# Optimization experiments

Measured on AMD Instinct MI355X. Metric: run time of the kernel, lower is better.

The kernel has to match this reference:

```python
import jax, jax.numpy as jnp
import numpy as np

N_NODES = 100000
N_EDGES = 1600000
N_GRAPHS = 512
F_IN = 20
HID = 128
OUT = HID // 2


def _glorot(key, shape):
    fan_in, fan_out = shape[0], shape[1]
    lim = float(np.sqrt(6.0 / (fan_in + fan_out)))
    return jax.random.uniform(key, shape, jnp.float32, -lim, lim)


def setup_inputs() -> dict:
    key = jax.random.key(0)
    ks = jax.random.split(key, 12)
    x = jax.random.normal(ks[0], (N_NODES, F_IN), jnp.float32)
    edge_index = jax.random.randint(ks[1], (2, N_EDGES), 0, N_NODES, dtype=jnp.int64)
    batch = jnp.sort(jax.random.randint(ks[2], (N_NODES,), 0, N_GRAPHS, dtype=jnp.int64))
    return {
        "x": x,
        "edge_index": edge_index,
        "batch": batch,
        "W1": _glorot(ks[3], (F_IN, HID)), "b1": jnp.zeros((HID,), jnp.float32),
        "W2": _glorot(ks[4], (HID, HID)), "b2": jnp.zeros((HID,), jnp.float32),
        "W3": _glorot(ks[5], (HID, HID)), "b3": jnp.zeros((HID,), jnp.float32),
        "Wout": _glorot(ks[6], (HID, OUT)), "bout": jnp.zeros((OUT,), jnp.float32),
    }


def _gcn_conv(x, W, b, src, dst, num_nodes):
    # PyG GCNConv: x' = D^{-1/2} (A + I) D^{-1/2} X W + b (self-loops already in src/dst)
    xw = x @ W                                                  # [N, H]
    ones = jnp.ones(src.shape[0], dtype=xw.dtype)
    deg = jax.ops.segment_sum(ones, dst, num_segments=num_nodes)
    dinv = jnp.where(deg > 0, jax.lax.rsqrt(deg), 0.0)          # [N]
    norm = dinv[src] * dinv[dst]                                # [E+N]
    msg = xw[src] * norm[:, None]                               # gather + scale
    return jax.ops.segment_sum(msg, dst, num_segments=num_nodes) + b


def reference(x, edge_index, batch, W1, b1, W2, b2, W3, b3, Wout, bout):
    num_nodes = x.shape[0]
    loops = jnp.arange(num_nodes, dtype=edge_index.dtype)
    src = jnp.concatenate([edge_index[0], loops])
    dst = jnp.concatenate([edge_index[1], loops])

    h = jax.nn.relu(_gcn_conv(x, W1, b1, src, dst, num_nodes))
    h = jax.nn.relu(_gcn_conv(h, W2, b2, src, dst, num_nodes))
    h = jax.nn.relu(_gcn_conv(h, W3, b3, src, dst, num_nodes))

    # global_mean_pool over graph ids
    sums = jax.ops.segment_sum(h, batch, num_segments=N_GRAPHS)
    counts = jax.ops.segment_sum(jnp.ones(num_nodes, h.dtype), batch, num_segments=N_GRAPHS)
    pooled = sums / jnp.maximum(counts, 1.0)[:, None]           # [G, H]
    return pooled @ Wout + bout                                 # [G, H//2]
```

## Files before the change

kernel.cpp:

```cpp
#include <hip/hip_runtime.h>
#include <hip/hip_fp16.h>

#define N_NODES 100000
#define N_EDGES 1600000
#define N_GRAPHS 512
#define F_IN 20
#define HID 128
#define OUT_F 64

#define BUCKETS 256
#define SPAN 391
#define BCAP 7000
#define EPB 2048

typedef _Float16 half8_t __attribute__((ext_vector_type(8)));
typedef float f32x4_t __attribute__((ext_vector_type(4)));

__device__ inline float4 h4_to_f4(uint2 u) {
    __half2 h0 = *(__half2*)&u.x;
    __half2 h1 = *(__half2*)&u.y;
    float2 f0 = __half22float2(h0);
    float2 f1 = __half22float2(h1);
    return make_float4(f0.x, f0.y, f1.x, f1.y);
}

__global__ void zero_all(float* sums, float* counts, int* cur256) {
    int i = blockIdx.x * 256 + threadIdx.x;
    sums[i] = 0.f;
    if (i < N_GRAPHS) counts[i] = 0.f;
    if (i >= 512 && i < 512 + BUCKETS) cur256[i - 512] = 0;
}

__global__ __launch_bounds__(256) void partition(const int* __restrict__ src,
                                                 const int* __restrict__ dst,
                                                 int* __restrict__ bpairs,
                                                 int* cur256) {
    __shared__ int lcnt[BUCKETS];
    __shared__ int lbase[BUCKETS];
    int t = threadIdx.x;
    lcnt[t] = 0;
    __syncthreads();
    int base = blockIdx.x * EPB;
    int myb[8], myp[8];
#pragma unroll
    for (int i = 0; i < 8; ++i) {
        int e = base + i * 256 + t;
        int b = -1, p = 0;
        if (e < N_EDGES) {
            int s = src[e], d = dst[e];
            b = d / SPAN;
            p = (s << 9) | (d - b * SPAN);
            atomicAdd(&lcnt[b], 1);
        }
        myb[i] = b; myp[i] = p;
    }
    __syncthreads();
    lbase[t] = atomicAdd(&cur256[t], lcnt[t]);
    lcnt[t] = 0;
    __syncthreads();
#pragma unroll
    for (int i = 0; i < 8; ++i) {
        int b = myb[i];
        if (b >= 0) {
            int p = lbase[b] + atomicAdd(&lcnt[b], 1);
            if (p < BCAP) bpairs[(size_t)b * BCAP + p] = myp[i];
        }
    }
}

__global__ void scan_bbase(const int* __restrict__ cur256, int* bbase, int* row_st) {
    __shared__ int sc[BUCKETS];
    int t = threadIdx.x;
    int v = cur256[t];
    sc[t] = v;
    __syncthreads();
    for (int o = 1; o < BUCKETS; o <<= 1) {
        int x = (t >= o) ? sc[t - o] : 0;
        __syncthreads();
        sc[t] += x;
        __syncthreads();
    }
    bbase[t] = sc[t] - v;
    if (t == 0) row_st[N_NODES] = N_EDGES;
}

__global__ __launch_bounds__(256) void csr_build(const int* __restrict__ bpairs,
                                                 const int* __restrict__ bcnt,
                                                 const int* __restrict__ bbase,
                                                 int* __restrict__ row_st,
                                                 int* __restrict__ csr) {
    __shared__ int ocnt[SPAN];
    __shared__ int sc[512];
    __shared__ int cur[SPAN];
    int b = blockIdx.x, t = threadIdx.x;
    int n0 = b * SPAN;
    int span = N_NODES - n0; if (span > SPAN) span = SPAN;
    for (int i = t; i < SPAN; i += 256) ocnt[i] = 0;
    __syncthreads();
    int n = bcnt[b];
    const int* p = bpairs + (size_t)b * BCAP;
    for (int i = t; i < n; i += 256) atomicAdd(&ocnt[p[i] & 511], 1);
    __syncthreads();
    sc[t]       = (t < span) ? ocnt[t] : 0;
    sc[t + 256] = (t + 256 < span) ? ocnt[t + 256] : 0;
    __syncthreads();
    for (int o = 1; o < 512; o <<= 1) {
        int a0 = (t >= o) ? sc[t - o] : 0;
        int a1 = sc[t + 256 - o];
        __syncthreads();
        sc[t] += a0;
        sc[t + 256] += a1;
        __syncthreads();
    }
    int base = bbase[b];
    for (int i = t; i < span; i += 256) {
        int start = sc[i] - ocnt[i];
        row_st[n0 + i] = base + start;
        cur[i] = start;
    }
    __syncthreads();
    for (int i = t; i < n; i += 256) {
        int e = p[i];
        int lp = atomicAdd(&cur[e & 511], 1);
        csr[base + lp] = e >> 9;
    }
}

__global__ void scale_x(const float* __restrict__ x, const int* __restrict__ row_st,
                        __half* __restrict__ Xs) {
    int i = blockIdx.x * 256 + threadIdx.x;
    int n = i >> 5, f = i & 31;
    if (n >= N_NODES) return;
    float v = (f < F_IN) ? x[n * F_IN + f] : 0.f;
    float di = rsqrtf((float)(row_st[n + 1] - row_st[n] + 1));
    Xs[i] = __float2half(di * v);
}

__global__ __launch_bounds__(256) void gather20(const __half* __restrict__ Xs,
                                                const int* __restrict__ row_st,
                                                const int* __restrict__ csr,
                                                float* __restrict__ Xagg) {
    int t = threadIdx.x;
    if (t >= 240) return;
    int g = t / F_IN, f = t % F_IN;
    int n = blockIdx.x * 12 + g;
    if (n >= N_NODES) return;
    int r0 = row_st[n], r1 = row_st[n + 1];
    float acc = __half2float(Xs[n * 32 + f]);
    int r = r0;
    for (; r + 3 < r1; r += 4) {
        int s0 = csr[r], s1 = csr[r + 1], s2 = csr[r + 2], s3 = csr[r + 3];
        float v0 = __half2float(Xs[s0 * 32 + f]);
        float v1 = __half2float(Xs[s1 * 32 + f]);
        float v2 = __half2float(Xs[s2 * 32 + f]);
        float v3 = __half2float(Xs[s3 * 32 + f]);
        acc += (v0 + v1) + (v2 + v3);
    }
    for (; r < r1; ++r) acc += __half2float(Xs[csr[r] * 32 + f]);
    float di = rsqrtf((float)(r1 - r0 + 1));
    Xagg[n * F_IN + f] = di * acc;
}

__global__ __launch_bounds__(256) void gemm_l1(const float* __restrict__ A,
                                               const float* __restrict__ W,
                                               const float* __restrict__ bias,
                                               __half* __restrict__ C) {
    __shared__ float Alds[16 * F_IN];
    __shared__ float Wlds[F_IN * HID];
    const int t = threadIdx.x;
    const int node0 = blockIdx.x * 16;

    for (int idx = t; idx < 16 * F_IN; idx += 256)
        Alds[idx] = A[node0 * F_IN + idx];
    for (int idx = t; idx < F_IN * HID; idx += 256)
        Wlds[idx] = W[idx];
    __syncthreads();

    const int h4 = (t & 31) * 4;
    const int g  = t >> 5;
    float4 b4 = *(const float4*)&bias[h4];
    float4 acc0 = b4;
    float4 acc1 = b4;
#pragma unroll
    for (int kk = 0; kk < F_IN; ++kk) {
        float a0 = Alds[(g * 2) * F_IN + kk];
        float a1 = Alds[(g * 2 + 1) * F_IN + kk];
        float4 w = *(const float4*)&Wlds[kk * HID + h4];
        acc0.x = fmaf(a0, w.x, acc0.x);
        acc0.y = fmaf(a0, w.y, acc0.y);
        acc0.z = fmaf(a0, w.z, acc0.z);
        acc0.w = fmaf(a0, w.w, acc0.w);
        acc1.x = fmaf(a1, w.x, acc1.x);
        acc1.y = fmaf(a1, w.y, acc1.y);
        acc1.z = fmaf(a1, w.z, acc1.z);
        acc1.w = fmaf(a1, w.w, acc1.w);
    }
    {
        __half2 h0 = __floats2half2_rn(acc0.x, acc0.y);
        __half2 h1 = __floats2half2_rn(acc0.z, acc0.w);
        uint2 u; u.x = *(unsigned*)&h0; u.y = *(unsigned*)&h1;
        ((uint2*)C)[(node0 + g * 2) * 32 + (h4 >> 2)] = u;
    }
    {
        __half2 h0 = __floats2half2_rn(acc1.x, acc1.y);
        __half2 h1 = __floats2half2_rn(acc1.z, acc1.w);
        uint2 u; u.x = *(unsigned*)&h0; u.y = *(unsigned*)&h1;
        ((uint2*)C)[(node0 + g * 2 + 1) * 32 + (h4 >> 2)] = u;
    }
}

__global__ __launch_bounds__(256) void gemm_mfma(const __half* __restrict__ H,
                                                 const float* __restrict__ W,
                                                 const int* __restrict__ row_st,
                                                 __half* __restrict__ T) {
    __shared__ _Float16 Whi[128 * 128];
    __shared__ _Float16 Wlo[128 * 128];
    const int t = threadIdx.x;

    for (int i = t; i < 128 * 128; i += 256) {
        int k = i >> 7, c = i & 127;
        float w = W[i];
        _Float16 hi = (_Float16)w;
        _Float16 lo = (_Float16)((w - (float)hi) * 2048.0f);
        int addr = c * 128 + (((k >> 3) ^ (c & 15)) << 3) + (k & 7);
        Whi[addr] = hi;
        Wlo[addr] = lo;
    }
    __syncthreads();

    const int wv = t >> 6;
    const int l  = t & 63;
    const int lr = l & 15;
    const int lq = l >> 4;

    for (int rep = 0; rep < 4; ++rep) {
        int strip = (blockIdx.x * 4 + wv) * 4 + rep;
        if (strip >= N_NODES / 16) continue;
        int n0 = strip * 16;

        f32x4_t acc[8], acl[8];
#pragma unroll
        for (int ct = 0; ct < 8; ++ct) { acc[ct] = (f32x4_t){0,0,0,0}; acl[ct] = (f32x4_t){0,0,0,0}; }

#pragma unroll
        for (int kc = 0; kc < 4; ++kc) {
            half8_t a = *(const half8_t*)(H + (size_t)(n0 + lr) * 128 + kc * 32 + lq * 8);
#pragma unroll
            for (int j = 0; j < 8; ++j) a[j] = a[j] > (_Float16)0 ? a[j] : (_Float16)0;
            int g = kc * 4 + lq;
#pragma unroll
            for (int ct = 0; ct < 8; ++ct) {
                int c = ct * 16 + lr;
                int addr = c * 128 + ((g ^ lr) << 3);
                half8_t bh = *(const half8_t*)&Whi[addr];
                half8_t bl = *(const half8_t*)&Wlo[addr];
                acc[ct] = __builtin_amdgcn_mfma_f32_16x16x32_f16(a, bh, acc[ct], 0, 0, 0);
                acl[ct] = __builtin_amdgcn_mfma_f32_16x16x32_f16(a, bl, acl[ct], 0, 0, 0);
            }
        }

        int r0 = n0 + lq * 4;
#pragma unroll
        for (int r = 0; r < 4; ++r) {
            int row = r0 + r;
            float d = rsqrtf((float)(row_st[row + 1] - row_st[row] + 1));
#pragma unroll
            for (int ct = 0; ct < 8; ++ct) {
                float v = (acc[ct][r] + acl[ct][r] * 4.8828125e-4f) * d;
                T[(size_t)row * 128 + ct * 16 + lr] = __float2half(v);
            }
        }
    }
}

__global__ __launch_bounds__(256) void gather_range(const __half* __restrict__ A,
                                                    const int* __restrict__ row_st,
                                                    const int* __restrict__ csr,
                                                    const float* __restrict__ bias,
                                                    __half* __restrict__ B) {
    int t = threadIdx.x;
    int n = blockIdx.x * 8 + (t >> 5);
    int l = t & 31;
    int r0 = row_st[n], r1 = row_st[n + 1];
    float di = rsqrtf((float)(r1 - r0 + 1));
    const uint2* Af = (const uint2*)A;
    float4 acc = h4_to_f4(Af[n * 32 + l]);
    int r = r0;
    for (; r + 3 < r1; r += 4) {
        int s0 = csr[r];
        int s1 = csr[r + 1];
        int s2 = csr[r + 2];
        int s3 = csr[r + 3];
        float4 v0 = h4_to_f4(Af[s0 * 32 + l]);
        float4 v1 = h4_to_f4(Af[s1 * 32 + l]);
        float4 v2 = h4_to_f4(Af[s2 * 32 + l]);
        float4 v3 = h4_to_f4(Af[s3 * 32 + l]);
        acc.x += (v0.x + v1.x) + (v2.x + v3.x);
        acc.y += (v0.y + v1.y) + (v2.y + v3.y);
        acc.z += (v0.z + v1.z) + (v2.z + v3.z);
        acc.w += (v0.w + v1.w) + (v2.w + v3.w);
    }
    for (; r < r1; ++r) {
        float4 v = h4_to_f4(Af[csr[r] * 32 + l]);
        acc.x += v.x; acc.y += v.y; acc.z += v.z; acc.w += v.w;
    }
    float4 b4 = ((const float4*)bias)[l];
    __half2 h0 = __floats2half2_rn(fmaf(di, acc.x, b4.x), fmaf(di, acc.y, b4.y));
    __half2 h1 = __floats2half2_rn(fmaf(di, acc.z, b4.z), fmaf(di, acc.w, b4.w));
    uint2 u; u.x = *(unsigned*)&h0; u.y = *(unsigned*)&h1;
    ((uint2*)B)[n * 32 + l] = u;
}

__global__ __launch_bounds__(256) void pool(const __half* __restrict__ B,
                                            const int* __restrict__ batch,
                                            float* sums, float* counts) {
    int t = threadIdx.x;
    int grp = blockIdx.x * 8 + (t >> 5);
    int l = t & 31;
    int h4 = l * 4;
    int n0 = grp * 8;
    if (n0 >= N_NODES) return;
    const uint2* Bf = (const uint2*)B;
    int cur = batch[n0];
    int runlen = 0;
    float4 acc = make_float4(0.f, 0.f, 0.f, 0.f);
    for (int k = 0; k < 8; ++k) {
        int n = n0 + k;
        if (n >= N_NODES) break;
        int g = batch[n];
        if (g != cur) {
            float* sp = &sums[cur * HID + h4];
            atomicAdd(sp + 0, acc.x); atomicAdd(sp + 1, acc.y);
            atomicAdd(sp + 2, acc.z); atomicAdd(sp + 3, acc.w);
            if (l == 0) atomicAdd(&counts[cur], (float)runlen);
            acc = make_float4(0.f, 0.f, 0.f, 0.f);
            runlen = 0;
            cur = g;
        }
        float4 v = h4_to_f4(Bf[n * 32 + l]);
        acc.x += fmaxf(v.x, 0.f);
        acc.y += fmaxf(v.y, 0.f);
        acc.z += fmaxf(v.z, 0.f);
        acc.w += fmaxf(v.w, 0.f);
        ++runlen;
    }
    float* sp = &sums[cur * HID + h4];
    atomicAdd(sp + 0, acc.x); atomicAdd(sp + 1, acc.y);
    atomicAdd(sp + 2, acc.z); atomicAdd(sp + 3, acc.w);
    if (l == 0) atomicAdd(&counts[cur], (float)runlen);
}

__global__ void final_gemm(const float* __restrict__ sums, const float* __restrict__ counts,
                           const float* __restrict__ Wout, const float* __restrict__ bout,
                           float* __restrict__ out) {
    int g = blockIdx.x;
    int o = threadIdx.x;
    __shared__ float p[HID];
    for (int k = o; k < HID; k += 64) p[k] = sums[g * HID + k];
    __syncthreads();
    float inv = 1.0f / fmaxf(counts[g], 1.0f);
    float acc = 0.f;
#pragma unroll 8
    for (int k = 0; k < HID; ++k)
        acc = fmaf(p[k], Wout[k * OUT_F + o], acc);
    out[g * OUT_F + o] = fmaf(inv, acc, bout[o]);
}

extern "C" void kernel_launch(void* const* d_in, const int* in_sizes, int n_in,
                              void* d_out, int out_size, void* d_ws, size_t ws_size,
                              hipStream_t stream) {
    const float* x     = (const float*)d_in[0];
    const int*   ei    = (const int*)d_in[1];
    const int*   batch = (const int*)d_in[2];
    const float* W1    = (const float*)d_in[3];
    const float* b1    = (const float*)d_in[4];
    const float* W2    = (const float*)d_in[5];
    const float* b2    = (const float*)d_in[6];
    const float* W3    = (const float*)d_in[7];
    const float* b3    = (const float*)d_in[8];
    const float* Wout  = (const float*)d_in[9];
    const float* bout  = (const float*)d_in[10];
    float* out = (float*)d_out;

    const int* src = ei;
    const int* dst = ei + N_EDGES;

    float* A      = (float*)d_ws;
    float* Breg   = A + (size_t)N_NODES * HID;
    int*   row_st = (int*)(Breg + (size_t)N_NODES * HID);
    float* sums   = (float*)(row_st + N_NODES + 1);
    float* counts = sums + N_GRAPHS * HID;
    int*   csr    = (int*)(counts + N_GRAPHS);
    int*   cur256 = csr + N_EDGES;
    int*   bbase  = cur256 + BUCKETS;

    int*    bpairs = (int*)A;
    __half* Xs     = (__half*)A;
    float*  Xagg   = A + 1600000;
    __half* T      = (__half*)A;
    __half* H      = (__half*)Breg;

    zero_all<<<N_GRAPHS * HID / 256, 256, 0, stream>>>(sums, counts, cur256);
    partition<<<(N_EDGES + EPB - 1) / EPB, 256, 0, stream>>>(src, dst, bpairs, cur256);
    scan_bbase<<<1, BUCKETS, 0, stream>>>(cur256, bbase, row_st);
    csr_build<<<BUCKETS, 256, 0, stream>>>(bpairs, cur256, bbase, row_st, csr);

    scale_x<<<N_NODES * 32 / 256, 256, 0, stream>>>(x, row_st, Xs);
    gather20<<<(N_NODES + 11) / 12, 256, 0, stream>>>(Xs, row_st, csr, Xagg);
    gemm_l1<<<N_NODES / 16, 256, 0, stream>>>(Xagg, W1, b1, H);

    gemm_mfma<<<391, 256, 0, stream>>>(H, W2, row_st, T);
    gather_range<<<N_NODES / 8, 256, 0, stream>>>(T, row_st, csr, b2, H);
    gemm_mfma<<<391, 256, 0, stream>>>(H, W3, row_st, T);
    gather_range<<<N_NODES / 8, 256, 0, stream>>>(T, row_st, csr, b3, H);

    pool<<<(N_NODES / 8 + 7) / 8, 256, 0, stream>>>(H, batch, sums, counts);
    final_gemm<<<N_GRAPHS, 64, 0, stream>>>(sums, counts, Wout, bout, out);
}
```

Measured before the change: 401.0 us.

## Fuse layer-1 gather into GEMM, per-wave partition counters, unroll gather by 8

Merges the 20-feature neighbor gather and the first-layer GEMM into one kernel, so the aggregated features stay in LDS and no longer round-trip through global memory. Partition now keeps a separate bucket counter per wavefront and takes each edge's rank from the first atomic, which removes the second pass of LDS atomics. The 128-wide gather loop is unrolled to 8 neighbors to put more loads in flight, and the zeroing kernel is replaced by hipMemsetAsync calls. The risks are higher register pressure from the unroll and a gather in layer1 that now uses 32 lanes per node while only 20 of them produce results.

```diff
diff --git a/kernel.cpp b/kernel.cpp
--- a/kernel.cpp
+++ b/kernel.cpp
@@ -24,45 +24,45 @@
     return make_float4(f0.x, f0.y, f1.x, f1.y);
 }
 
-__global__ void zero_all(float* sums, float* counts, int* cur256) {
-    int i = blockIdx.x * 256 + threadIdx.x;
-    sums[i] = 0.f;
-    if (i < N_GRAPHS) counts[i] = 0.f;
-    if (i >= 512 && i < 512 + BUCKETS) cur256[i - 512] = 0;
-}
-
 __global__ __launch_bounds__(256) void partition(const int* __restrict__ src,
                                                  const int* __restrict__ dst,
                                                  int* __restrict__ bpairs,
                                                  int* cur256) {
-    __shared__ int lcnt[BUCKETS];
-    __shared__ int lbase[BUCKETS];
+    __shared__ int lcnt[4][BUCKETS];
+    __shared__ int woff[4][BUCKETS];
     int t = threadIdx.x;
-    lcnt[t] = 0;
+    int wv = t >> 6;
+    for (int i = t; i < 4 * BUCKETS; i += 256) ((int*)lcnt)[i] = 0;
     __syncthreads();
     int base = blockIdx.x * EPB;
-    int myb[8], myp[8];
+    int myb[8], myp[8], myr[8];
 #pragma unroll
     for (int i = 0; i < 8; ++i) {
         int e = base + i * 256 + t;
-        int b = -1, p = 0;
+        int b = -1, p = 0, rk = 0;
         if (e < N_EDGES) {
             int s = src[e], d = dst[e];
             b = d / SPAN;
             p = (s << 9) | (d - b * SPAN);
-            atomicAdd(&lcnt[b], 1);
-        }
-        myb[i] = b; myp[i] = p;
-    }
-    __syncthreads();
-    lbase[t] = atomicAdd(&cur256[t], lcnt[t]);
-    lcnt[t] = 0;
+            rk = atomicAdd(&lcnt[wv][b], 1);
+        }
+        myb[i] = b; myp[i] = p; myr[i] = rk;
+    }
+    __syncthreads();
+    {
+        int c0 = lcnt[0][t], c1 = lcnt[1][t], c2 = lcnt[2][t], c3 = lcnt[3][t];
+        int gb = atomicAdd(&cur256[t], c0 + c1 + c2 + c3);
+        woff[0][t] = gb;
+        woff[1][t] = gb + c0;
+        woff[2][t] = gb + c0 + c1;
+        woff[3][t] = gb + c0 + c1 + c2;
+    }
     __syncthreads();
 #pragma unroll
     for (int i = 0; i < 8; ++i) {
         int b = myb[i];
         if (b >= 0) {
-            int p = lbase[b] + atomicAdd(&lcnt[b], 1);
+            int p = woff[wv][b] + myr[i];
             if (p < BCAP) bpairs[(size_t)b * BCAP + p] = myp[i];
         }
     }
@@ -136,44 +136,37 @@
     Xs[i] = __float2half(di * v);
 }
 
-__global__ __launch_bounds__(256) void gather20(const __half* __restrict__ Xs,
-                                                const int* __restrict__ row_st,
-                                                const int* __restrict__ csr,
-                                                float* __restrict__ Xagg) {
-    int t = threadIdx.x;
-    if (t >= 240) return;
-    int g = t / F_IN, f = t % F_IN;
-    int n = blockIdx.x * 12 + g;
-    if (n >= N_NODES) return;
-    int r0 = row_st[n], r1 = row_st[n + 1];
-    float acc = __half2float(Xs[n * 32 + f]);
-    int r = r0;
-    for (; r + 3 < r1; r += 4) {
-        int s0 = csr[r], s1 = csr[r + 1], s2 = csr[r + 2], s3 = csr[r + 3];
-        float v0 = __half2float(Xs[s0 * 32 + f]);
-        float v1 = __half2float(Xs[s1 * 32 + f]);
-        float v2 = __half2float(Xs[s2 * 32 + f]);
-        float v3 = __half2float(Xs[s3 * 32 + f]);
-        acc += (v0 + v1) + (v2 + v3);
-    }
-    for (; r < r1; ++r) acc += __half2float(Xs[csr[r] * 32 + f]);
-    float di = rsqrtf((float)(r1 - r0 + 1));
-    Xagg[n * F_IN + f] = di * acc;
-}
-
-__global__ __launch_bounds__(256) void gemm_l1(const float* __restrict__ A,
-                                               const float* __restrict__ W,
-                                               const float* __restrict__ bias,
-                                               __half* __restrict__ C) {
+__global__ __launch_bounds__(256) void layer1(const __half* __restrict__ Xs,
+                                              const int* __restrict__ row_st,
+                                              const int* __restrict__ csr,
+                                              const float* __restrict__ W,
+                                              const float* __restrict__ bias,
+                                              __half* __restrict__ H) {
+    __shared__ float Wlds[F_IN * HID];
     __shared__ float Alds[16 * F_IN];
-    __shared__ float Wlds[F_IN * HID];
     const int t = threadIdx.x;
     const int node0 = blockIdx.x * 16;
 
-    for (int idx = t; idx < 16 * F_IN; idx += 256)
-        Alds[idx] = A[node0 * F_IN + idx];
-    for (int idx = t; idx < F_IN * HID; idx += 256)
-        Wlds[idx] = W[idx];
+    for (int i = t; i < F_IN * HID; i += 256) Wlds[i] = W[i];
+
+    const int hw = t >> 5, l = t & 31;
+    for (int k = 0; k < 2; ++k) {
+        int nn = node0 + hw * 2 + k;
+        int r0 = row_st[nn], r1 = row_st[nn + 1];
+        float acc = __half2float(Xs[nn * 32 + l]);
+        int r = r0;
+        for (; r + 3 < r1; r += 4) {
+            int s0 = csr[r], s1 = csr[r + 1], s2 = csr[r + 2], s3 = csr[r + 3];
+            float v0 = __half2float(Xs[s0 * 32 + l]);
+            float v1 = __half2float(Xs[s1 * 32 + l]);
+            float v2 = __half2float(Xs[s2 * 32 + l]);
+            float v3 = __half2float(Xs[s3 * 32 + l]);
+            acc += (v0 + v1) + (v2 + v3);
+        }
+        for (; r < r1; ++r) acc += __half2float(Xs[csr[r] * 32 + l]);
+        float di = rsqrtf((float)(r1 - r0 + 1));
+        if (l < F_IN) Alds[(hw * 2 + k) * F_IN + l] = di * acc;
+    }
     __syncthreads();
 
     const int h4 = (t & 31) * 4;
@@ -199,13 +192,13 @@
         __half2 h0 = __floats2half2_rn(acc0.x, acc0.y);
         __half2 h1 = __floats2half2_rn(acc0.z, acc0.w);
         uint2 u; u.x = *(unsigned*)&h0; u.y = *(unsigned*)&h1;
-        ((uint2*)C)[(node0 + g * 2) * 32 + (h4 >> 2)] = u;
+        ((uint2*)H)[(node0 + g * 2) * 32 + (h4 >> 2)] = u;
     }
     {
         __half2 h0 = __floats2half2_rn(acc1.x, acc1.y);
         __half2 h1 = __floats2half2_rn(acc1.z, acc1.w);
         uint2 u; u.x = *(unsigned*)&h0; u.y = *(unsigned*)&h1;
-        ((uint2*)C)[(node0 + g * 2 + 1) * 32 + (h4 >> 2)] = u;
+        ((uint2*)H)[(node0 + g * 2 + 1) * 32 + (h4 >> 2)] = u;
     }
 }
 
@@ -286,11 +279,24 @@
     const uint2* Af = (const uint2*)A;
     float4 acc = h4_to_f4(Af[n * 32 + l]);
     int r = r0;
+    for (; r + 7 < r1; r += 8) {
+        int s0 = csr[r],     s1 = csr[r + 1], s2 = csr[r + 2], s3 = csr[r + 3];
+        int s4 = csr[r + 4], s5 = csr[r + 5], s6 = csr[r + 6], s7 = csr[r + 7];
+        float4 v0 = h4_to_f4(Af[s0 * 32 + l]);
+        float4 v1 = h4_to_f4(Af[s1 * 32 + l]);
+        float4 v2 = h4_to_f4(Af[s2 * 32 + l]);
+        float4 v3 = h4_to_f4(Af[s3 * 32 + l]);
+        float4 v4 = h4_to_f4(Af[s4 * 32 + l]);
+        float4 v5 = h4_to_f4(Af[s5 * 32 + l]);
+        float4 v6 = h4_to_f4(Af[s6 * 32 + l]);
+        float4 v7 = h4_to_f4(Af[s7 * 32 + l]);
+        acc.x += ((v0.x + v1.x) + (v2.x + v3.x)) + ((v4.x + v5.x) + (v6.x + v7.x));
+        acc.y += ((v0.y + v1.y) + (v2.y + v3.y)) + ((v4.y + v5.y) + (v6.y + v7.y));
+        acc.z += ((v0.z + v1.z) + (v2.z + v3.z)) + ((v4.z + v5.z) + (v6.z + v7.z));
+        acc.w += ((v0.w + v1.w) + (v2.w + v3.w)) + ((v4.w + v5.w) + (v6.w + v7.w));
+    }
     for (; r + 3 < r1; r += 4) {
-        int s0 = csr[r];
-        int s1 = csr[r + 1];
-        int s2 = csr[r + 2];
-        int s3 = csr[r + 3];
+        int s0 = csr[r], s1 = csr[r + 1], s2 = csr[r + 2], s3 = csr[r + 3];
         float4 v0 = h4_to_f4(Af[s0 * 32 + l]);
         float4 v1 = h4_to_f4(Af[s1 * 32 + l]);
         float4 v2 = h4_to_f4(Af[s2 * 32 + l]);
@@ -396,18 +402,17 @@
 
     int*    bpairs = (int*)A;
     __half* Xs     = (__half*)A;
-    float*  Xagg   = A + 1600000;
     __half* T      = (__half*)A;
     __half* H      = (__half*)Breg;
 
-    zero_all<<<N_GRAPHS * HID / 256, 256, 0, stream>>>(sums, counts, cur256);
+    hipMemsetAsync(sums, 0, (N_GRAPHS * HID + N_GRAPHS) * sizeof(float), stream);
+    hipMemsetAsync(cur256, 0, BUCKETS * sizeof(int), stream);
     partition<<<(N_EDGES + EPB - 1) / EPB, 256, 0, stream>>>(src, dst, bpairs, cur256);
     scan_bbase<<<1, BUCKETS, 0, stream>>>(cur256, bbase, row_st);
     csr_build<<<BUCKETS, 256, 0, stream>>>(bpairs, cur256, bbase, row_st, csr);
 
     scale_x<<<N_NODES * 32 / 256, 256, 0, stream>>>(x, row_st, Xs);
-    gather20<<<(N_NODES + 11) / 12, 256, 0, stream>>>(Xs, row_st, csr, Xagg);
-    gemm_l1<<<N_NODES / 16, 256, 0, stream>>>(Xagg, W1, b1, H);
+    layer1<<<N_NODES / 16, 256, 0, stream>>>(Xs, row_st, csr, W1, b1, H);
 
     gemm_mfma<<<391, 256, 0, stream>>>(H, W2, row_st, T);
     gather_range<<<N_NODES / 8, 256, 0, stream>>>(T, row_st, csr, b2, H);
```

Result: slower. 411.7 us (+2.7%).
